# Optimization experiments

Measured on AMD Instinct MI355X. Metric: run time of the kernel, lower is better.

The kernel has to match this reference:

```python
import jax, jax.numpy as jnp
import numpy as np

B, S, D, H, K = 1, 4096, 1024, 16, 64


def setup_inputs() -> dict:
    key = jax.random.key(0)
    ks = jax.random.split(key, 5)
    x = jax.random.normal(ks[0], (B, S, D), dtype=jnp.float32)
    wq = jax.random.normal(ks[1], (D, H, K), dtype=jnp.float32) / np.sqrt(D)
    wk = jax.random.normal(ks[2], (D, H, K), dtype=jnp.float32) / np.sqrt(D)
    wv = jax.random.normal(ks[3], (D, H, K), dtype=jnp.float32) / np.sqrt(D)
    wo = jax.random.normal(ks[4], (H, K, D), dtype=jnp.float32) / np.sqrt(H * K)
    bq = jnp.zeros((H, K), dtype=jnp.float32)
    bk = jnp.zeros((H, K), dtype=jnp.float32)
    bv = jnp.zeros((H, K), dtype=jnp.float32)
    bo = jnp.zeros((D,), dtype=jnp.float32)
    return {"x": x, "wq": wq, "bq": bq, "wk": wk, "bk": bk,
            "wv": wv, "bv": bv, "wo": wo, "bo": bo, "is_causal": 1}


def reference(x, wq, bq, wk, bk, wv, bv, wo, bo, is_causal):
    # QKV projections: [B,S,D] x [D,H,K] -> [B,S,H,K]
    q = jnp.einsum("bsd,dhk->bshk", x, wq) + bq
    k = jnp.einsum("bsd,dhk->bshk", x, wk) + bk
    v = jnp.einsum("bsd,dhk->bshk", x, wv) + bv
    # scores: [B,H,Q,KV], scaled by 1/sqrt(head_dim)
    scores = jnp.einsum("bqhk,bvhk->bhqv", q, k) / jnp.sqrt(jnp.float32(K))
    if is_causal:
        qpos = jnp.arange(S)[:, None]  # query position
        kpos = jnp.arange(S)[None, :]  # key position
        mask = (qpos >= kpos).astype(scores.dtype)  # [Q,KV]
        scores = scores - 1e9 * (1.0 - mask)
    probs = jax.nn.softmax(scores, axis=-1)
    # weighted values: [B,S,H,K]
    vals = jnp.einsum("bhqv,bvhk->bqhk", probs, v)
    # output projection: [B,S,H,K] x [H,K,D] -> [B,S,D]
    out = jnp.einsum("bqhk,hkd->bqd", vals, wo) + bo
    return out
```

## Files before the change

### kernel.cpp

```cpp
#include <hip/hip_runtime.h>

typedef _Float16 f16;
typedef f16 f16x8 __attribute__((ext_vector_type(8)));
typedef f16 f16x4 __attribute__((ext_vector_type(4)));
typedef float f32x4 __attribute__((ext_vector_type(4)));
typedef float f32x16 __attribute__((ext_vector_type(16)));
typedef unsigned u32;

#define MFMA16(a, b, c) __builtin_amdgcn_mfma_f32_16x16x32_f16((a), (b), (c), 0, 0, 0)
#define MFMA32(a, b, c) __builtin_amdgcn_mfma_f32_32x32x16_f16((a), (b), (c), 0, 0, 0)

#define QSCL 0.18033688011f

#define WAITV(N) asm volatile("s_waitcnt vmcnt(" #N ")" ::: "memory")
#define BAR()                          \
  {                                    \
    __builtin_amdgcn_s_barrier();      \
    __builtin_amdgcn_sched_barrier(0); \
  }

__device__ __forceinline__ void gll16(const void* g, void* l) {
  __builtin_amdgcn_global_load_lds(
      (__attribute__((address_space(1))) unsigned int*)(void*)(g),
      (__attribute__((address_space(3))) unsigned int*)(l), 16, 0, 0);
}

__device__ __forceinline__ float ex2(float x) {
  float r;
  asm("v_exp_f32 %0, %1" : "=v"(r) : "v"(x));
  return r;
}

__device__ __forceinline__ void plswap(u32& a, u32& b) {
  asm("s_nop 1\n\tv_permlane32_swap_b32 %0, %1\n\ts_nop 1" : "+v"(a), "+v"(b));
}

__device__ __forceinline__ u32 pk16(float lo, float hi) {
  __fp16 h2[2];
  *(decltype(__builtin_amdgcn_cvt_pkrtz(0.f, 0.f))*)h2 =
      __builtin_amdgcn_cvt_pkrtz(lo, hi);
  return *(u32*)h2;
}

__global__ void k_prep(const float* __restrict__ x, f16* __restrict__ xb,
                       const float* __restrict__ wq, const float* __restrict__ wk,
                       const float* __restrict__ wv, const float* __restrict__ wo,
                       f16* __restrict__ wqkvT, f16* __restrict__ woT) {
  __shared__ float tile[64][65];
  const int bid = blockIdx.x;
  if (bid < 4096) {
    const int i = bid * 256 + threadIdx.x;
    float4 v = reinterpret_cast<const float4*>(x)[i];
    f16x4 o = {(f16)v.x, (f16)v.y, (f16)v.z, (f16)v.w};
    reinterpret_cast<f16x4*>(xb)[i] = o;
    return;
  }
  const int tb = bid - 4096;
  const int which = tb >> 8;
  const int bidx = tb & 255;
  const float* src = which == 0 ? wq : which == 1 ? wk : which == 2 ? wv : wo;
  f16* dst = which == 0 ? wqkvT
             : which == 1 ? wqkvT + (size_t)1024 * 1024
             : which == 2 ? wqkvT + (size_t)2048 * 1024
                          : woT;
  const int bc = bidx & 15, br = bidx >> 4;
  const int r0 = br << 6, c0 = bc << 6;
  const int tr = threadIdx.x >> 6, tc = threadIdx.x & 63;
#pragma unroll
  for (int p = 0; p < 16; ++p)
    tile[p * 4 + tr][tc] = src[(size_t)(r0 + p * 4 + tr) * 1024 + c0 + tc];
  __syncthreads();
#pragma unroll
  for (int p = 0; p < 16; ++p)
    dst[(size_t)(c0 + p * 4 + tr) * 1024 + r0 + tc] = (f16)tile[tc][p * 4 + tr];
}

template <int MODE, int NFR, int PAIR>
__global__ __launch_bounds__(256, 3) void k_gemm(
    const f16* __restrict__ A, const f16* __restrict__ Bt, int nbm, int Kd,
    const float* __restrict__ bias0, const float* __restrict__ bias1,
    const float* __restrict__ bias2,
    f16* __restrict__ Qo, f16* __restrict__ Ko, f16* __restrict__ Vo,
    float* __restrict__ Fo) {
  constexpr int TSZ = 8192 + NFR * 2048;
  constexpr int NBUF = PAIR ? 4 : 3;
  __shared__ __align__(16) char smem[NBUF * TSZ];
  const int tid = threadIdx.x;
  const int wid = tid >> 6, lane = tid & 63;
  const int r = lane & 15, t = lane >> 4;
  const int bm = blockIdx.x % nbm, bn = blockIdx.x / nbm;
  const int m0 = bm << 7, n0 = bn * (NFR * 32);
  const int wr = wid >> 1, wc = wid & 1;

  const f32x4 vz = {0.f, 0.f, 0.f, 0.f};
  f32x4 acc[4][NFR];
#pragma unroll
  for (int m = 0; m < 4; ++m)
#pragma unroll
    for (int n = 0; n < NFR; ++n) acc[m][n] = vz;

  const int srow = tid >> 2;
  const int scb = (((tid & 3) ^ ((tid >> 3) & 3)) << 4);
  const size_t ldb = (size_t)Kd * 2;
  const char* Ab = (const char*)A + (size_t)m0 * ldb + scb;
  const char* Bb = (const char*)Bt + (size_t)n0 * ldb + scb;

  auto issue = [&](int kt, int buf) {
    const size_t kb = (size_t)kt << 6;
    char* base = smem + buf * TSZ;
    gll16(Ab + (size_t)srow * ldb + kb, base + wid * 1024);
    gll16(Ab + (size_t)(srow + 64) * ldb + kb, base + 4096 + wid * 1024);
    gll16(Bb + (size_t)srow * ldb + kb, base + 8192 + wid * 1024);
    if (NFR == 4)
      gll16(Bb + (size_t)(srow + 64) * ldb + kb, base + 8192 + 4096 + wid * 1024);
  };

  const int swz = ((r >> 1) & 3) << 4;

  auto comp = [&](int buf) {
    const char* base = smem + buf * TSZ;
    f16x8 af[4], bg[NFR];
#pragma unroll
    for (int m = 0; m < 4; ++m)
      af[m] = *(const f16x8*)(base + ((wr * 64 + m * 16 + r) * 64 +
                                      ((t * 16) ^ swz)));
#pragma unroll
    for (int n = 0; n < NFR; ++n)
      bg[n] = *(const f16x8*)(base + 8192 +
                              ((wc * (NFR * 16) + n * 16 + r) * 64 +
                               ((t * 16) ^ swz)));
    __builtin_amdgcn_s_setprio(1);
#pragma unroll
    for (int m = 0; m < 4; ++m)
#pragma unroll
      for (int n = 0; n < NFR; ++n) acc[m][n] = MFMA16(af[m], bg[n], acc[m][n]);
    __builtin_amdgcn_s_setprio(0);
  };

  const int nk = Kd >> 5;
  if (PAIR) {
    issue(0, 0);
    issue(1, 1);
    const int nsup = nk >> 1;
    for (int T = 0; T < nsup; ++T) {
      WAITV(0);
      BAR();
      if (T + 1 < nsup) {
        issue(2 * T + 2, (2 * T + 2) & 3);
        issue(2 * T + 3, (2 * T + 3) & 3);
      }
      comp((2 * T) & 3);
      comp((2 * T + 1) & 3);
    }
  } else {
    issue(0, 0);
    issue(1, 1);
    int b = 0, bi = 2;
    for (int kt = 0; kt < nk; ++kt) {
      if (kt + 1 < nk) {
        if (NFR == 4) {
          WAITV(4);
        } else {
          WAITV(3);
        }
      } else {
        WAITV(0);
      }
      BAR();
      if (kt + 2 < nk) issue(kt + 2, bi);
      comp(b);
      b = (b == 2) ? 0 : b + 1;
      bi = (bi == 2) ? 0 : bi + 1;
    }
  }

#pragma unroll
  for (int m = 0; m < 4; ++m) {
    const int row0 = m0 + wr * 64 + m * 16 + t * 4;
#pragma unroll
    for (int n = 0; n < NFR; ++n) {
      const int gc = n0 + wc * (NFR * 16) + n * 16 + r;
      if (MODE == 0) {
        const float b2 = gc < 1024 ? bias0[gc]
                                   : (gc < 2048 ? bias1[gc - 1024] : bias2[gc - 2048]);
        float v[4];
#pragma unroll
        for (int i = 0; i < 4; ++i) v[i] = acc[m][n][i] + b2;
        if (gc < 1024) {
#pragma unroll
          for (int i = 0; i < 4; ++i)
            Qo[(size_t)(row0 + i) * 1024 + gc] = (f16)(v[i] * QSCL);
        } else if (gc < 2048) {
#pragma unroll
          for (int i = 0; i < 4; ++i)
            Ko[(size_t)(row0 + i) * 1024 + (gc - 1024)] = (f16)v[i];
        } else {
          f16x4 pk = {(f16)v[0], (f16)v[1], (f16)v[2], (f16)v[3]};
          *(f16x4*)(Vo + (size_t)(gc - 2048) * 4096 + row0) = pk;
        }
      } else {
        const float b2 = bias0[gc];
#pragma unroll
        for (int i = 0; i < 4; ++i)
          Fo[(size_t)(row0 + i) * 1024 + gc] = acc[m][n][i] + b2;
      }
    }
  }
}

__constant__ unsigned char g_qt[48] = {
    15, 30, 31, 31, 14, 28, 29, 29, 30, 13, 26, 27, 27, 28, 12, 24,
    25, 25, 26, 11, 22, 23, 23, 24, 10, 20, 21, 21, 22, 9,  18, 19,
    19, 20, 8,  16, 17, 17, 18, 7,  16, 6,  5,  4,  3,  2,  1,  0};
__constant__ unsigned char g_ch[48] = {
    2, 0, 0, 1, 2, 0, 0, 1, 1, 2, 0, 0, 1, 1, 2, 0,
    0, 1, 1, 2, 0, 0, 1, 1, 2, 0, 0, 1, 1, 2, 0, 0,
    1, 1, 2, 0, 0, 1, 1, 2, 1, 2, 2, 2, 2, 2, 2, 2};

__global__ __launch_bounds__(512, 4) void k_fattn(
    const f16* __restrict__ Q, const f16* __restrict__ Kb,
    const f16* __restrict__ Vt, f16* __restrict__ vals,
    const int* __restrict__ causp, f16* __restrict__ part_o,
    float* __restrict__ part_ls) {
  __shared__ uint4 ldsv[4128];
  char* lds = (char*)ldsv;
  const int tid = threadIdx.x;
  const int W = tid >> 6, lane = tid & 63;
  const int l31 = lane & 31, hi = lane >> 5;
  const int wq = W >> 1, wkv = W & 1;
  const int h = blockIdx.x & 15;
  const int it = blockIdx.x >> 4;
  const int qt = g_qt[it];
  const int ch = g_ch[it];
  const int cz = *causp;
  int Tstart, tlen;
  if (ch == 2) {
    Tstart = 0;
    tlen = cz ? qt + 1 : 32;
  } else if (ch == 0) {
    Tstart = 0;
    tlen = cz ? (qt + 2) >> 1 : 16;
  } else {
    Tstart = cz ? (qt + 2) >> 1 : 16;
    tlen = cz ? (qt + 1) >> 1 : 16;
  }
  const int Tend = Tstart + tlen - 1;
  const int dw = wq - wkv;
  const int jmax_w = cz ? (2 * qt + (dw >= 2 ? 1 : 0) - (dw < 0 ? 1 : 0)) : 63;
  const bool maskd = cz && ((dw & 1) == 0);

  const size_t qrow = (size_t)((qt << 7) + (wq << 5) + l31) * 1024 + h * 64;
  f16x8 qf[4];
#pragma unroll
  for (int s = 0; s < 4; ++s) qf[s] = *(const f16x8*)(Q + qrow + 16 * s + 8 * hi);

  f32x16 o0, o1, zv;
#pragma unroll
  for (int e = 0; e < 16; ++e) { o0[e] = 0.f; o1[e] = 0.f; zv[e] = 0.f; }
  float Ls = 0.f;

  const int srw = lane >> 3, sch = lane & 7;
  const int ssw = (sch ^ srw) << 3;
  const char* kcur =
      (const char*)(Kb + (size_t)(8 * W + srw) * 1024 + h * 64 + ssw) +
      (size_t)Tstart * 262144;
  const char* vcur =
      (const char*)(Vt + (size_t)(h * 64 + 8 * W + srw) * 4096 + ssw) +
      (size_t)Tstart * 256;

  auto issue = [&](int buf) {
    char* base = lds + buf * 16384 + W * 1024;
    gll16(kcur, base);
    gll16(vcur, base + 8192);
    kcur += (size_t)64 * 2048;
    vcur += 128;
  };

  const int krow = (wkv << 5) + l31, ksw = krow & 7;
  const int vsw = l31 & 7;

  auto qk = [&](const char* Kbase) -> f32x16 {
    f16x8 af[4];
#pragma unroll
    for (int s = 0; s < 4; ++s)
      af[s] = *(const f16x8*)(Kbase + krow * 128 + (((2 * s + hi) ^ ksw) << 4));
    __builtin_amdgcn_s_setprio(1);
    f32x16 sc = MFMA32(af[0], qf[0], zv);
#pragma unroll
    for (int s = 1; s < 4; ++s) sc = MFMA32(af[s], qf[s], sc);
    __builtin_amdgcn_s_setprio(0);
    return sc;
  };

  auto fin = [&](int j, const char* Kbase, f32x16& sc) {
    const char* Vbase = Kbase + 8192;
    if (maskd && j == jmax_w) {
#pragma unroll
      for (int e = 0; e < 16; ++e) {
        const int kvr = (e & 3) + 8 * (e >> 2) + 4 * hi;
        if (kvr > l31) sc[e] = -1e9f;
      }
    }
    float p[16];
#pragma unroll
    for (int e = 0; e < 16; ++e) p[e] = ex2(sc[e]);
    {
      float s0 = (p[0] + p[1]) + (p[2] + p[3]);
      float s1 = (p[4] + p[5]) + (p[6] + p[7]);
      float s2 = (p[8] + p[9]) + (p[10] + p[11]);
      float s3 = (p[12] + p[13]) + (p[14] + p[15]);
      float s = (s0 + s1) + (s2 + s3);
      union { float f; u32 u; } ua, ub;
      ua.f = s; ub.f = s;
      plswap(ua.u, ub.u);
      Ls += ua.f + ub.f;
    }
#pragma unroll
    for (int ks = 0; ks < 2; ++ks) {
      u32 c0 = pk16(p[8 * ks + 0], p[8 * ks + 1]);
      u32 c1 = pk16(p[8 * ks + 2], p[8 * ks + 3]);
      u32 c2 = pk16(p[8 * ks + 4], p[8 * ks + 5]);
      u32 c3 = pk16(p[8 * ks + 6], p[8 * ks + 7]);
      plswap(c0, c2);
      plswap(c1, c3);
      union { u32 w[4]; f16x8 v; } pa;
      pa.w[0] = c0; pa.w[1] = c1; pa.w[2] = c2; pa.w[3] = c3;
      const int cl = 4 * wkv + 2 * ks + hi;
      const f16x8 vf0 = *(const f16x8*)(Vbase + l31 * 128 + ((cl ^ vsw) << 4));
      const f16x8 vf1 =
          *(const f16x8*)(Vbase + (32 + l31) * 128 + ((cl ^ vsw) << 4));
      __builtin_amdgcn_s_setprio(1);
      o0 = MFMA32(pa.v, vf0, o0);
      o1 = MFMA32(pa.v, vf1, o1);
      __builtin_amdgcn_s_setprio(0);
    }
  };

  {
    const int pb = 2 * (Tstart & 1);
    issue(pb);
    issue(pb + 1);
  }

  for (int T = Tstart; T <= Tend; ++T) {
    BAR();
    if (T < Tend) {
      const int nb = 2 * ((T + 1) & 1);
      issue(nb);
      issue(nb + 1);
      WAITV(4);
    } else {
      WAITV(0);
    }
    const int cb = 2 * (T & 1);
    const char* bA = lds + cb * 16384;
    const char* bB = lds + (cb + 1) * 16384;
    const int jA = 2 * T, jB = 2 * T + 1;
    if (jB <= jmax_w) {
      f32x16 scA = qk(bA);
      f32x16 scB = qk(bB);
      fin(jA, bA, scA);
      fin(jB, bB, scB);
    } else if (jA <= jmax_w) {
      f32x16 scA = qk(bA);
      fin(jA, bA, scA);
    }
  }
  __syncthreads();

  float* obuf = (float*)lds;
  float* lsbuf = (float*)(lds + 32768);
  if (hi == 0) lsbuf[wq * 64 + wkv * 32 + l31] = Ls;
  if (wkv == 1) {
    float* base = obuf + wq * 2048;
#pragma unroll
    for (int dblk = 0; dblk < 2; ++dblk)
#pragma unroll
      for (int rg = 0; rg < 4; ++rg) {
        const f32x16& o = dblk ? o1 : o0;
        f32x4 t = {o[rg * 4 + 0], o[rg * 4 + 1], o[rg * 4 + 2], o[rg * 4 + 3]};
        *(f32x4*)(base + ((dblk * 4 + rg) * 64 + lane) * 4) = t;
      }
  }
  __syncthreads();

  float lst[16];
  const bool writer = (wkv == 0);
  if (writer) {
    float* base = obuf + wq * 2048;
#pragma unroll
    for (int dblk = 0; dblk < 2; ++dblk)
#pragma unroll
      for (int rg = 0; rg < 4; ++rg) {
        f32x4 t = *(f32x4*)(base + ((dblk * 4 + rg) * 64 + lane) * 4);
        f32x16& o = dblk ? o1 : o0;
#pragma unroll
        for (int i = 0; i < 4; ++i) o[rg * 4 + i] += t[i];
      }
#pragma unroll
    for (int e = 0; e < 16; ++e) {
      const int q = (e & 3) + 8 * (e >> 2) + 4 * hi;
      lst[e] = lsbuf[wq * 64 + q] + lsbuf[wq * 64 + 32 + q];
    }
  }

  if (ch == 2) {
    if (writer) {
      const int row0 = (qt << 7) + (wq << 5);
#pragma unroll
      for (int dblk = 0; dblk < 2; ++dblk) {
        const f32x16& o = dblk ? o1 : o0;
        const int col = h * 64 + 32 * dblk + l31;
#pragma unroll
        for (int e = 0; e < 16; ++e) {
          const int rr = row0 + (e & 3) + 8 * (e >> 2) + 4 * hi;
          vals[(size_t)rr * 1024 + col] = (f16)(o[e] / lst[e]);
        }
      }
    }
    return;
  }

  if (writer) {
    const int tix = h * 16 + (qt - 16);
    const int slot = (tix << 1) | ch;
    f16* po = part_o + (size_t)slot * 8192;
    float* pl = part_ls + slot * 128;
#pragma unroll
    for (int dblk = 0; dblk < 2; ++dblk) {
      const f32x16& o = dblk ? o1 : o0;
      const int col = 32 * dblk + l31;
#pragma unroll
      for (int e = 0; e < 16; ++e) {
        const int rr = 32 * wq + (e & 3) + 8 * (e >> 2) + 4 * hi;
        po[rr * 64 + col] = (f16)o[e];
      }
    }
    if (l31 == 0) {
#pragma unroll
      for (int e = 0; e < 16; ++e) {
        const int q = (e & 3) + 8 * (e >> 2) + 4 * hi;
        pl[32 * wq + q] = lst[e];
      }
    }
  }
}

__global__ __launch_bounds__(256) void k_fix(const f16* __restrict__ part_o,
                                             const float* __restrict__ part_ls,
                                             f16* __restrict__ vals) {
  const int tix = blockIdx.x;
  const int h = tix >> 4, qt = 16 + (tix & 15);
  const int t = threadIdx.x;
  const int row = t >> 1, c0 = (t & 1) * 32;
  const f16* po0 = part_o + (((size_t)tix << 1) | 0) * 8192;
  const f16* po1 = part_o + (((size_t)tix << 1) | 1) * 8192;
  const float ls = part_ls[((tix << 1) | 0) * 128 + row] +
                   part_ls[((tix << 1) | 1) * 128 + row];
  const float inv = 1.0f / ls;
  const f16* a = po0 + row * 64 + c0;
  const f16* b = po1 + row * 64 + c0;
  f16* d = vals + (size_t)((qt << 7) + row) * 1024 + h * 64 + c0;
#pragma unroll
  for (int i = 0; i < 4; ++i) {
    f16x8 va = *(const f16x8*)(a + 8 * i);
    f16x8 vb = *(const f16x8*)(b + 8 * i);
    f16x8 vo;
#pragma unroll
    for (int j = 0; j < 8; ++j)
      vo[j] = (f16)(((float)va[j] + (float)vb[j]) * inv);
    *(f16x8*)(d + 8 * i) = vo;
  }
}

extern "C" void kernel_launch(void* const* d_in, const int* in_sizes, int n_in,
                              void* d_out, int out_size, void* d_ws, size_t ws_size,
                              hipStream_t stream) {
  const float* x = (const float*)d_in[0];
  const float* wq = (const float*)d_in[1];
  const float* bq = (const float*)d_in[2];
  const float* wk = (const float*)d_in[3];
  const float* bk = (const float*)d_in[4];
  const float* wv = (const float*)d_in[5];
  const float* bv = (const float*)d_in[6];
  const float* wo = (const float*)d_in[7];
  const float* bo = (const float*)d_in[8];
  const int* caus = (const int*)d_in[9];
  float* out = (float*)d_out;

  f16* xb = (f16*)d_ws;
  f16* wqkvT = xb + (size_t)4096 * 1024;
  f16* woT = wqkvT + (size_t)3072 * 1024;
  f16* Qb = woT + (size_t)1024 * 1024;
  f16* Kbuf = Qb + (size_t)4096 * 1024;
  f16* Vt = Kbuf + (size_t)4096 * 1024;
  f16* vals = Vt + (size_t)4096 * 1024;

  f16* part_o = xb;
  float* part_ls = (float*)wqkvT;

  k_prep<<<5120, 256, 0, stream>>>(x, xb, wq, wk, wv, wo, wqkvT, woT);
  k_gemm<0, 4, 0><<<32 * 24, 256, 0, stream>>>(xb, wqkvT, 32, 1024, bq, bk, bv,
                                               Qb, Kbuf, Vt, nullptr);
  k_fattn<<<768, 512, 0, stream>>>(Qb, Kbuf, Vt, vals, caus, part_o, part_ls);
  k_fix<<<256, 256, 0, stream>>>(part_o, part_ls, vals);
  k_gemm<1, 2, 1><<<32 * 16, 256, 0, stream>>>(vals, woT, 32, 1024, bo, nullptr,
                                               nullptr, nullptr, nullptr,
                                               nullptr, out);
}
```

Before: 120.4 us.

## Switch attention K/V staging to a triple-buffered single-tile pipeline for occupancy

The flash-attention kernel now streams one 64-row K/V tile per iteration through three rotating LDS buffers, replacing the earlier double-buffered pairs of tiles. This cuts the static LDS footprint from about 66KB to about 50KB, and the launch bound is raised from 4 to 6 so more blocks can be resident per CU. The QK^T and PV steps are merged into one per-tile routine, with K fragment loads interleaved between the MFMAs. The cost is that two tiles' QK MFMAs can no longer be interleaved, and the tighter launch bound may constrain registers or cause spills.

```diff
diff --git a/kernel.cpp b/kernel.cpp
--- a/kernel.cpp
+++ b/kernel.cpp
@@ -217,12 +217,12 @@
     0, 1, 1, 2, 0, 0, 1, 1, 2, 0, 0, 1, 1, 2, 0, 0,
     1, 1, 2, 0, 0, 1, 1, 2, 1, 2, 2, 2, 2, 2, 2, 2};
 
-__global__ __launch_bounds__(512, 4) void k_fattn(
+__global__ __launch_bounds__(512, 6) void k_fattn(
     const f16* __restrict__ Q, const f16* __restrict__ Kb,
     const f16* __restrict__ Vt, f16* __restrict__ vals,
     const int* __restrict__ causp, f16* __restrict__ part_o,
     float* __restrict__ part_ls) {
-  __shared__ uint4 ldsv[4128];
+  __shared__ uint4 ldsv[3136];
   char* lds = (char*)ldsv;
   const int tid = threadIdx.x;
   const int W = tid >> 6, lane = tid & 63;
@@ -244,7 +244,8 @@
     Tstart = cz ? (qt + 2) >> 1 : 16;
     tlen = cz ? (qt + 1) >> 1 : 16;
   }
-  const int Tend = Tstart + tlen - 1;
+  const int j0 = 2 * Tstart;
+  const int n = 2 * tlen - 1;
   const int dw = wq - wkv;
   const int jmax_w = cz ? (2 * qt + (dw >= 2 ? 1 : 0) - (dw < 0 ? 1 : 0)) : 63;
   const bool maskd = cz && ((dw & 1) == 0);
@@ -263,10 +264,10 @@
   const int ssw = (sch ^ srw) << 3;
   const char* kcur =
       (const char*)(Kb + (size_t)(8 * W + srw) * 1024 + h * 64 + ssw) +
-      (size_t)Tstart * 262144;
+      (size_t)j0 * 131072;
   const char* vcur =
       (const char*)(Vt + (size_t)(h * 64 + 8 * W + srw) * 4096 + ssw) +
-      (size_t)Tstart * 256;
+      (size_t)j0 * 128;
 
   auto issue = [&](int buf) {
     char* base = lds + buf * 16384 + W * 1024;
@@ -279,21 +280,20 @@
   const int krow = (wkv << 5) + l31, ksw = krow & 7;
   const int vsw = l31 & 7;
 
-  auto qk = [&](const char* Kbase) -> f32x16 {
-    f16x8 af[4];
-#pragma unroll
-    for (int s = 0; s < 4; ++s)
-      af[s] = *(const f16x8*)(Kbase + krow * 128 + (((2 * s + hi) ^ ksw) << 4));
+  auto tilec = [&](int j, const char* Kbase) {
+    if (j > jmax_w) return;
+    const char* Vbase = Kbase + 8192;
     __builtin_amdgcn_s_setprio(1);
-    f32x16 sc = MFMA32(af[0], qf[0], zv);
-#pragma unroll
-    for (int s = 1; s < 4; ++s) sc = MFMA32(af[s], qf[s], sc);
+    const f16x8 af0 =
+        *(const f16x8*)(Kbase + krow * 128 + ((hi ^ ksw) << 4));
+    f32x16 sc = MFMA32(af0, qf[0], zv);
+#pragma unroll
+    for (int s = 1; s < 4; ++s) {
+      const f16x8 af =
+          *(const f16x8*)(Kbase + krow * 128 + (((2 * s + hi) ^ ksw) << 4));
+      sc = MFMA32(af, qf[s], sc);
+    }
     __builtin_amdgcn_s_setprio(0);
-    return sc;
-  };
-
-  auto fin = [&](int j, const char* Kbase, f32x16& sc) {
-    const char* Vbase = Kbase + 8192;
     if (maskd && j == jmax_w) {
 #pragma unroll
       for (int e = 0; e < 16; ++e) {
@@ -336,40 +336,25 @@
     }
   };
 
-  {
-    const int pb = 2 * (Tstart & 1);
-    issue(pb);
-    issue(pb + 1);
-  }
-
-  for (int T = Tstart; T <= Tend; ++T) {
+  issue(0);
+  issue(1);
+
+  for (int jj = 0; jj <= n; ++jj) {
     BAR();
-    if (T < Tend) {
-      const int nb = 2 * ((T + 1) & 1);
-      issue(nb);
-      issue(nb + 1);
+    if (jj + 2 <= n) {
+      issue((jj + 2) % 3);
       WAITV(4);
+    } else if (jj + 1 <= n) {
+      WAITV(2);
     } else {
       WAITV(0);
     }
-    const int cb = 2 * (T & 1);
-    const char* bA = lds + cb * 16384;
-    const char* bB = lds + (cb + 1) * 16384;
-    const int jA = 2 * T, jB = 2 * T + 1;
-    if (jB <= jmax_w) {
-      f32x16 scA = qk(bA);
-      f32x16 scB = qk(bB);
-      fin(jA, bA, scA);
-      fin(jB, bB, scB);
-    } else if (jA <= jmax_w) {
-      f32x16 scA = qk(bA);
-      fin(jA, bA, scA);
-    }
+    tilec(j0 + jj, lds + (jj % 3) * 16384);
   }
   __syncthreads();
 
   float* obuf = (float*)lds;
-  float* lsbuf = (float*)(lds + 32768);
+  float* lsbuf = (float*)(lds + 49152);
   if (hi == 0) lsbuf[wq * 64 + wkv * 32 + l31] = Ls;
   if (wkv == 1) {
     float* base = obuf + wq * 2048;
```

Result: slower. 162.9 us (+35.3%).
